# Kernel tuning notes

Measured on AMD Instinct MI355X. Metric: run time of the kernel, lower is better.

The kernel has to match this reference:

```python
import jax, jax.numpy as jnp
import numpy as np

B, C, H, W = 64, 512, 8, 8
K = 100            # num_class
H1, HID, L = 64, 128, 32   # ae_hidden[0], fixed hidd, ae_latent
CLIP = 100.0       # CSSRClassifier.clip_len
RED = -0.1         # model='pcssr' -> -1, times gamma=0.1
PUSH_THRESH = 10000.0


def setup_inputs() -> dict:
    key = jax.random.key(0)
    ks = jax.random.split(key, 9)
    s = lambda fan_in: 1.0 / np.sqrt(fan_in)  # kaiming-ish 1x1 conv init scale
    return {
        "x": jax.random.normal(ks[0], (B, C, H, W), jnp.float32),
        "ycls": jax.random.randint(ks[1], (B,), 0, K),
        "safe_margin_all": jax.random.normal(ks[2], (K,), jnp.float32),
        "safe_distance_all": jax.random.normal(ks[3], (K,), jnp.float32),
        "W1": jax.random.normal(ks[4], (K, H1, C), jnp.float32) * s(C),
        "W2": jax.random.normal(ks[5], (K, HID, H1), jnp.float32) * s(H1),
        "W3": jax.random.normal(ks[6], (K, L, HID), jnp.float32) * s(HID),
        "prototypes": jax.random.normal(ks[7], (K, L, H, W), jnp.float32),
        "prototypes1": jax.random.normal(ks[8], (K, L, H, W), jnp.float32),
    }


def reference(x, ycls, safe_margin_all, safe_distance_all, W1, W2, W3, prototypes, prototypes1):
    P = H * W
    xf = x.reshape(B, C, P)
    # per-class 1x1-conv encoder (tanh after every conv), batched over classes k
    h = jnp.tanh(jnp.einsum('koc,bcp->kbop', W1, xf))      # [K,B,H1,P]
    h = jnp.tanh(jnp.einsum('koi,kbip->kbop', W2, h))      # [K,B,HID,P]
    lt = jnp.tanh(jnp.einsum('koi,kbip->kbop', W3, h))     # [K,B,L,P]
    p = prototypes.reshape(K, 1, L, P)
    p1 = prototypes1.reshape(K, 1, L, P)
    # squared-L2 distance over channel dim, scaled by reduction, clipped
    er = jnp.clip(jnp.sum((lt - p) ** 2, axis=2) * RED, -CLIP, CLIP)    # [K,B,P]
    er1 = jnp.clip(jnp.sum((lt - p1) ** 2, axis=2) * RED, -CLIP, CLIP)  # [K,B,P]
    # training losses (pull on er1, push on er), vectorized across classes
    f = jnp.sum(er, axis=2)    # [K,B] spatial-summed errors
    f1 = jnp.sum(er1, axis=2)  # [K,B]
    cls_ids = jnp.arange(K)[:, None]
    mask_eq = (ycls[None, :] == cls_ids).astype(f.dtype)   # [K,B]
    n_eq = jnp.sum(mask_eq, axis=1)
    pull = jnp.sum(jnp.where(n_eq > 0,
                             jnp.sum(f1 * mask_eq, axis=1) / jnp.maximum(n_eq, 1.0),
                             0.0))
    comb = (1.0 - mask_eq) * (f < PUSH_THRESH).astype(f.dtype)
    n_comb = jnp.sum(comb, axis=1)
    push = jnp.sum(jnp.where(n_comb > 0,
                             jnp.sum(f * comb, axis=1) / jnp.maximum(n_comb, 1.0),
                             0.0))
    # cat per-class [B,1,H,W] errors along dim 1 -> [B,K,H,W]
    logits = jnp.transpose(er, (1, 0, 2)).reshape(B, K, H, W)
    logits1 = jnp.transpose(er1, (1, 0, 2)).reshape(B, K, H, W)
    return logits, logits1, pull, push
```

## Files before the change

kernel.cpp:

```cpp
#include <hip/hip_runtime.h>

typedef short  s16x8  __attribute__((ext_vector_type(8)));
typedef float  f32x16 __attribute__((ext_vector_type(16)));
typedef unsigned short u16;
typedef unsigned long long u64b;

#define MFMA32(a,b,c) __builtin_amdgcn_mfma_f32_32x32x16_bf16((a),(b),(c),0,0,0)
#define KCLS 100

__device__ __forceinline__ u16 f2bf(float f) {
  return (u16)(__builtin_bit_cast(unsigned, f) >> 16);
}

__device__ __forceinline__ float tanh_fast(float x) {
  float e = __builtin_amdgcn_exp2f(x * 2.8853900817779268f);
  return 1.0f - 2.0f * __builtin_amdgcn_rcpf(e + 1.0f);
}

__device__ __forceinline__ void ld_lds16(const void* g, void* l) {
  __builtin_amdgcn_global_load_lds(
      (const __attribute__((address_space(1))) unsigned char*)g,
      (__attribute__((address_space(3))) unsigned char*)l, 16, 0, 0);
}

__global__ void prep(const float* __restrict__ x, const float* __restrict__ w1,
                     const float* __restrict__ w2, const float* __restrict__ w3,
                     u16* __restrict__ xF, u16* __restrict__ W1F,
                     u16* __restrict__ W2F, u16* __restrict__ W3F,
                     float* __restrict__ fz, float* __restrict__ out2) {
  __shared__ float tile[64][65];
  const int bid = blockIdx.x, t = threadIdx.x;
  if (bid == 0 && t < 2) out2[t] = 0.f;
  if (bid < 512) {
    const int b = bid >> 3, ck = bid & 7;
    #pragma unroll
    for (int j = 0; j < 4; j++) {
      int e4 = j * 1024 + t * 4;
      int c = e4 >> 6, p0 = e4 & 63;
      float4 v = *(const float4*)(x + ((size_t)b * 512 + ck * 64 + c) * 64 + p0);
      tile[c][p0] = v.x; tile[c][p0 + 1] = v.y; tile[c][p0 + 2] = v.z; tile[c][p0 + 3] = v.w;
    }
    __syncthreads();
    #pragma unroll
    for (int i = 0; i < 2; i++) {
      int s = i * 256 + t;
      int ksl = s >> 7, ph = (s >> 6) & 1, lane = s & 63;
      int cb = ksl * 16 + (lane >> 5) * 8, pp = ph * 32 + (lane & 31);
      u16 o[8];
      #pragma unroll
      for (int jj = 0; jj < 8; jj++) o[jj] = f2bf(tile[cb + jj][pp]);
      *(uint4*)(xF + (((size_t)b * 64 + (ck * 4 + ksl) * 2 + ph) * 512) + lane * 8) = *(uint4*)o;
    }
  } else if (bid < 1312) {
    int base = (bid - 512) * 512;
    #pragma unroll
    for (int i = 0; i < 2; i++) {
      int s = base + i * 256 + t;
      int frag = s >> 6, lane = s & 63;
      int k = frag >> 6, fr = frag & 63;
      int m = (fr & 1) * 32 + (lane & 31);
      int c0 = (fr >> 1) * 16 + (lane >> 5) * 8;
      const float* src = w1 + ((size_t)k * 64 + m) * 512 + c0;
      float4 a = *(const float4*)src, b4 = *(const float4*)(src + 4);
      u16 o[8] = { f2bf(a.x), f2bf(a.y), f2bf(a.z), f2bf(a.w),
                   f2bf(b4.x), f2bf(b4.y), f2bf(b4.z), f2bf(b4.w) };
      *(uint4*)(W1F + ((size_t)frag * 512) + lane * 8) = *(uint4*)o;
    }
  } else if (bid < 1512) {
    int base = (bid - 1312) * 512;
    #pragma unroll
    for (int i = 0; i < 2; i++) {
      int s = base + i * 256 + t;
      int frag = s >> 6, lane = s & 63;
      int k = frag >> 4, fr = frag & 15;
      int m = (fr & 3) * 32 + (lane & 31);
      int c0 = (fr >> 2) * 16 + (lane >> 5) * 8;
      const float* src = w2 + ((size_t)k * 128 + m) * 64 + c0;
      float4 a = *(const float4*)src, b4 = *(const float4*)(src + 4);
      u16 o[8] = { f2bf(a.x), f2bf(a.y), f2bf(a.z), f2bf(a.w),
                   f2bf(b4.x), f2bf(b4.y), f2bf(b4.z), f2bf(b4.w) };
      *(uint4*)(W2F + ((size_t)frag * 512) + lane * 8) = *(uint4*)o;
    }
  } else if (bid < 1612) {
    int base = (bid - 1512) * 512;
    #pragma unroll
    for (int i = 0; i < 2; i++) {
      int s = base + i * 256 + t;
      int frag = s >> 6, lane = s & 63;
      int k = frag >> 3, kb = frag & 7;
      int m = lane & 31;
      int c0 = kb * 16 + (lane >> 5) * 8;
      const float* src = w3 + ((size_t)k * 32 + m) * 128 + c0;
      float4 a = *(const float4*)src, b4 = *(const float4*)(src + 4);
      u16 o[8] = { f2bf(a.x), f2bf(a.y), f2bf(a.z), f2bf(a.w),
                   f2bf(b4.x), f2bf(b4.y), f2bf(b4.z), f2bf(b4.w) };
      *(uint4*)(W3F + ((size_t)frag * 512) + lane * 8) = *(uint4*)o;
    }
  } else {
    int i4 = (bid - 1612) * 256 + t;
    if (i4 < 3200) {
      float4 z = {0.f, 0.f, 0.f, 0.f};
      *(float4*)(fz + (size_t)i4 * 4) = z;
    }
  }
}

__global__ __launch_bounds__(256, 4) void cssr_main(
    const u16* __restrict__ W1F, const u16* __restrict__ W2F, const u16* __restrict__ W3F,
    const u16* __restrict__ xF, const float* __restrict__ protos,
    const float* __restrict__ protos1, float* __restrict__ out,
    float* __restrict__ fw, float* __restrict__ f1w)
{
  __shared__ u16 pool[16384];

  const int bid = blockIdx.x;
  const int kp = bid >> 6, b = bid & 63;
  const int tid = threadIdx.x, w = tid >> 6, lane = tid & 63;
  const int nhalf = lane >> 5, nn = lane & 31;
  const int kk = w >> 1, mt = w & 1;
  const int k = kp * 2 + kk;

  const u16* xb = xF + ((size_t)b * 64) * 512;

  #pragma unroll
  for (int i = 0; i < 4; i++) {
    int f = w * 4 + i, gksl = f >> 1, ph = f & 1;
    ld_lds16(xb + ((size_t)(gksl * 2 + ph)) * 512 + lane * 8, &pool[f * 512]);
  }
  __syncthreads();

  f32x16 acc1[2] = {};
  for (int ci = 0; ci < 4; ci++) {
    const int pb = ci & 1;
    if (ci < 3) {
      #pragma unroll
      for (int i = 0; i < 4; i++) {
        int f = w * 4 + i, gksl = f >> 1, ph = f & 1;
        ld_lds16(xb + ((size_t)(((ci + 1) * 8 + gksl) * 2 + ph)) * 512 + lane * 8,
                 &pool[(pb ^ 1) * 8192 + f * 512]);
      }
    }
    #pragma unroll
    for (int ksl = 0; ksl < 8; ksl++) {
      s16x8 A = *(const s16x8*)(W1F + (((size_t)k * 64 + (ci * 8 + ksl) * 2 + mt) * 512) + lane * 8);
      #pragma unroll
      for (int nt = 0; nt < 2; nt++) {
        s16x8 B = *(const s16x8*)&pool[pb * 8192 + (ksl * 2 + nt) * 512 + lane * 8];
        acc1[nt] = MFMA32(A, B, acc1[nt]);
      }
    }
    __syncthreads();
  }

  #pragma unroll
  for (int nt = 0; nt < 2; nt++) {
    #pragma unroll
    for (int g = 0; g < 4; g++) {
      u16 hv[4];
      #pragma unroll
      for (int q = 0; q < 4; q++) hv[q] = f2bf(tanh_fast(acc1[nt][g * 4 + q]));
      int kb = mt * 2 + (g >> 1);
      int tl = (g & 1) * 32 + nn;
      *(u64b*)&pool[kk * 4096 + (kb * 2 + nt) * 512 + tl * 8 + nhalf * 4] = *(u64b*)hv;
    }
  }
  __syncthreads();

  f32x16 acc2[2][2] = {};
  #pragma unroll
  for (int kb = 0; kb < 4; kb++) {
    s16x8 A0 = *(const s16x8*)(W2F + (((size_t)k * 16 + kb * 4 + mt * 2 + 0) * 512) + lane * 8);
    s16x8 A1 = *(const s16x8*)(W2F + (((size_t)k * 16 + kb * 4 + mt * 2 + 1) * 512) + lane * 8);
    #pragma unroll
    for (int nh = 0; nh < 2; nh++) {
      s16x8 B = *(const s16x8*)&pool[kk * 4096 + (kb * 2 + nh) * 512 + lane * 8];
      acc2[0][nh] = MFMA32(A0, B, acc2[0][nh]);
      acc2[1][nh] = MFMA32(A1, B, acc2[1][nh]);
    }
  }
  __syncthreads();

  #pragma unroll
  for (int m4l = 0; m4l < 2; m4l++) {
    #pragma unroll
    for (int nh = 0; nh < 2; nh++) {
      #pragma unroll
      for (int g = 0; g < 4; g++) {
        u16 hv[4];
        #pragma unroll
        for (int q = 0; q < 4; q++) hv[q] = f2bf(tanh_fast(acc2[m4l][nh][g * 4 + q]));
        int kb2 = mt * 4 + m4l * 2 + (g >> 1);
        int tl  = (g & 1) * 32 + nn;
        *(u64b*)&pool[kk * 8192 + (kb2 * 2 + nh) * 512 + tl * 8 + nhalf * 4] = *(u64b*)hv;
      }
    }
  }
  __syncthreads();

  f32x16 acc3 = {};
  #pragma unroll
  for (int kb = 0; kb < 8; kb++) {
    s16x8 A = *(const s16x8*)(W3F + (((size_t)k * 8 + kb) * 512) + lane * 8);
    s16x8 B = *(const s16x8*)&pool[kk * 8192 + (kb * 2 + mt) * 512 + lane * 8];
    acc3 = MFMA32(A, B, acc3);
  }

  const int p = mt * 32 + nn;
  const float* pr  = protos  + (size_t)k * 2048;
  const float* pr1 = protos1 + (size_t)k * 2048;
  float d2 = 0.f, d21 = 0.f;
  #pragma unroll
  for (int g = 0; g < 4; g++) {
    #pragma unroll
    for (int q = 0; q < 4; q++) {
      int m = q + 8 * g + 4 * nhalf;
      float lt = tanh_fast(acc3[g * 4 + q]);
      float d = lt - pr [m * 64 + p];  d2  += d * d;
      float e = lt - pr1[m * 64 + p];  d21 += e * e;
    }
  }
  d2 += __shfl_xor(d2, 32); d21 += __shfl_xor(d21, 32);
  float er  = fminf(fmaxf(d2  * -0.1f, -100.f), 100.f);
  float er1 = fminf(fmaxf(d21 * -0.1f, -100.f), 100.f);
  if (nhalf == 0) {
    out[(size_t)b * 6400 + k * 64 + p]          = er;
    out[409600 + (size_t)b * 6400 + k * 64 + p] = er1;
  }
  float s = er, s1 = er1;
  s += __shfl_xor(s, 1);  s1 += __shfl_xor(s1, 1);
  s += __shfl_xor(s, 2);  s1 += __shfl_xor(s1, 2);
  s += __shfl_xor(s, 4);  s1 += __shfl_xor(s1, 4);
  s += __shfl_xor(s, 8);  s1 += __shfl_xor(s1, 8);
  s += __shfl_xor(s, 16); s1 += __shfl_xor(s1, 16);
  if (lane == 0) {
    atomicAdd(&fw [k * 64 + b], s);
    atomicAdd(&f1w[k * 64 + b], s1);
  }
}

__global__ void finalize(const float* __restrict__ f, const float* __restrict__ f1,
                         const int* __restrict__ ycls, float* __restrict__ out2) {
  const int k = blockIdx.x, b = threadIdx.x;
  float fv = f[k * 64 + b], f1v = f1[k * 64 + b];
  bool eq = (ycls[b] == k);
  bool cb = (!eq) && (fv < 10000.f);
  float s1 = eq ? f1v : 0.f, ne = eq ? 1.f : 0.f;
  float s  = cb ? fv  : 0.f, nc = cb ? 1.f : 0.f;
  #pragma unroll
  for (int o = 1; o < 64; o <<= 1) {
    s1 += __shfl_xor(s1, o); ne += __shfl_xor(ne, o);
    s  += __shfl_xor(s,  o); nc += __shfl_xor(nc, o);
  }
  if (b == 0) {
    if (ne > 0.f) atomicAdd(&out2[0], s1 / ne);
    if (nc > 0.f) atomicAdd(&out2[1], s / nc);
  }
}

extern "C" void kernel_launch(void* const* d_in, const int* in_sizes, int n_in,
                              void* d_out, int out_size, void* d_ws, size_t ws_size,
                              hipStream_t stream) {
  const float* x     = (const float*)d_in[0];
  const int*   ycls  = (const int*)d_in[1];
  const float* W1    = (const float*)d_in[4];
  const float* W2    = (const float*)d_in[5];
  const float* W3    = (const float*)d_in[6];
  const float* prot  = (const float*)d_in[7];
  const float* prot1 = (const float*)d_in[8];
  float* out = (float*)d_out;

  char* ws = (char*)d_ws;
  u16*  xFb = (u16*)(ws);
  u16*  W1F = (u16*)(ws + 4194304);
  u16*  W2F = (u16*)(ws + 10747904);
  u16*  W3F = (u16*)(ws + 12386304);
  float* fw  = (float*)(ws + 13205504);
  float* f1w = (float*)(ws + 13231104);

  prep<<<1625, 256, 0, stream>>>(x, W1, W2, W3, xFb, W1F, W2F, W3F,
                                 fw, out + 819200);
  cssr_main<<<50 * 64, 256, 0, stream>>>(W1F, W2F, W3F, xFb, prot, prot1,
                                         out, fw, f1w);
  finalize<<<KCLS, 64, 0, stream>>>(fw, f1w, ycls, out + 819200);
}
```

Before: 146.8 us.

## Keep inter-layer activations in registers via permlane32 swap, drop LDS staging

The main kernel is restructured so each wave owns one class, one batch item and half the spatial positions. The tanh outputs of layers 1 and 2 are packed to bf16 and rearranged into MFMA B-operand fragments with v_permlane32_swap, replacing the LDS round-trips and the block barriers between layers. The x tile is now read straight from global memory instead of being double-buffered through LDS, and the grid becomes 100x32 blocks. In exchange, W1 and x fragments are re-read from global/L2 by more waves, and register pressure rises.

After: 150.7 us. 1.03x slower.

```diff
diff --git a/kernel.cpp b/kernel.cpp
--- a/kernel.cpp
+++ b/kernel.cpp
@@ -3,6 +3,7 @@
 typedef short  s16x8  __attribute__((ext_vector_type(8)));
 typedef float  f32x16 __attribute__((ext_vector_type(16)));
 typedef unsigned short u16;
+typedef unsigned int   u32;
 typedef unsigned long long u64b;
 
 #define MFMA32(a,b,c) __builtin_amdgcn_mfma_f32_32x32x16_bf16((a),(b),(c),0,0,0)
@@ -10,17 +11,15 @@
 
 __device__ __forceinline__ u16 f2bf(float f) {
   return (u16)(__builtin_bit_cast(unsigned, f) >> 16);
+}
+
+__device__ __forceinline__ u32 pk2bf(float lo, float hi) {
+  return (__builtin_bit_cast(u32, lo) >> 16) | (__builtin_bit_cast(u32, hi) & 0xffff0000u);
 }
 
 __device__ __forceinline__ float tanh_fast(float x) {
   float e = __builtin_amdgcn_exp2f(x * 2.8853900817779268f);
   return 1.0f - 2.0f * __builtin_amdgcn_rcpf(e + 1.0f);
-}
-
-__device__ __forceinline__ void ld_lds16(const void* g, void* l) {
-  __builtin_amdgcn_global_load_lds(
-      (const __attribute__((address_space(1))) unsigned char*)g,
-      (__attribute__((address_space(3))) unsigned char*)l, 16, 0, 0);
 }
 
 __global__ void prep(const float* __restrict__ x, const float* __restrict__ w1,
@@ -105,124 +104,91 @@
   }
 }
 
+template<int GG>
+__device__ __forceinline__ s16x8 mk_bfrag(const f32x16 a) {
+  u32 P0 = pk2bf(tanh_fast(a[8 * GG + 0]), tanh_fast(a[8 * GG + 1]));
+  u32 P1 = pk2bf(tanh_fast(a[8 * GG + 2]), tanh_fast(a[8 * GG + 3]));
+  u32 Q0 = pk2bf(tanh_fast(a[8 * GG + 4]), tanh_fast(a[8 * GG + 5]));
+  u32 Q1 = pk2bf(tanh_fast(a[8 * GG + 6]), tanh_fast(a[8 * GG + 7]));
+  asm("v_permlane32_swap_b32 %0, %1" : "+v"(P0), "+v"(Q0));
+  asm("v_permlane32_swap_b32 %0, %1" : "+v"(P1), "+v"(Q1));
+  int4 wv = { (int)P0, (int)P1, (int)Q0, (int)Q1 };
+  return __builtin_bit_cast(s16x8, wv);
+}
+
 __global__ __launch_bounds__(256, 4) void cssr_main(
     const u16* __restrict__ W1F, const u16* __restrict__ W2F, const u16* __restrict__ W3F,
     const u16* __restrict__ xF, const float* __restrict__ protos,
     const float* __restrict__ protos1, float* __restrict__ out,
     float* __restrict__ fw, float* __restrict__ f1w)
 {
-  __shared__ u16 pool[16384];
-
   const int bid = blockIdx.x;
-  const int kp = bid >> 6, b = bid & 63;
+  const int k = bid >> 5, bp = bid & 31;
   const int tid = threadIdx.x, w = tid >> 6, lane = tid & 63;
-  const int nhalf = lane >> 5, nn = lane & 31;
-  const int kk = w >> 1, mt = w & 1;
-  const int k = kp * 2 + kk;
-
-  const u16* xb = xF + ((size_t)b * 64) * 512;
-
-  #pragma unroll
-  for (int i = 0; i < 4; i++) {
-    int f = w * 4 + i, gksl = f >> 1, ph = f & 1;
-    ld_lds16(xb + ((size_t)(gksl * 2 + ph)) * 512 + lane * 8, &pool[f * 512]);
-  }
-  __syncthreads();
+  const int bq = w >> 1, ph = w & 1;
+  const int b = bp * 2 + bq;
+  const int h = lane >> 5, nn = lane & 31;
+
+  const u16* xb  = xF  + ((size_t)b * 64) * 512 + lane * 8;
+  const u16* Wk1 = W1F + ((size_t)k * 64) * 512 + lane * 8;
 
   f32x16 acc1[2] = {};
-  for (int ci = 0; ci < 4; ci++) {
-    const int pb = ci & 1;
-    if (ci < 3) {
-      #pragma unroll
-      for (int i = 0; i < 4; i++) {
-        int f = w * 4 + i, gksl = f >> 1, ph = f & 1;
-        ld_lds16(xb + ((size_t)(((ci + 1) * 8 + gksl) * 2 + ph)) * 512 + lane * 8,
-                 &pool[(pb ^ 1) * 8192 + f * 512]);
-      }
-    }
-    #pragma unroll
-    for (int ksl = 0; ksl < 8; ksl++) {
-      s16x8 A = *(const s16x8*)(W1F + (((size_t)k * 64 + (ci * 8 + ksl) * 2 + mt) * 512) + lane * 8);
-      #pragma unroll
-      for (int nt = 0; nt < 2; nt++) {
-        s16x8 B = *(const s16x8*)&pool[pb * 8192 + (ksl * 2 + nt) * 512 + lane * 8];
-        acc1[nt] = MFMA32(A, B, acc1[nt]);
-      }
-    }
-    __syncthreads();
-  }
-
-  #pragma unroll
-  for (int nt = 0; nt < 2; nt++) {
-    #pragma unroll
-    for (int g = 0; g < 4; g++) {
-      u16 hv[4];
-      #pragma unroll
-      for (int q = 0; q < 4; q++) hv[q] = f2bf(tanh_fast(acc1[nt][g * 4 + q]));
-      int kb = mt * 2 + (g >> 1);
-      int tl = (g & 1) * 32 + nn;
-      *(u64b*)&pool[kk * 4096 + (kb * 2 + nt) * 512 + tl * 8 + nhalf * 4] = *(u64b*)hv;
-    }
-  }
-  __syncthreads();
-
-  f32x16 acc2[2][2] = {};
+  #pragma unroll
+  for (int ksl = 0; ksl < 32; ksl++) {
+    s16x8 B  = *(const s16x8*)(xb  + (ksl * 2 + ph) * 512);
+    s16x8 A0 = *(const s16x8*)(Wk1 + (ksl * 2 + 0) * 512);
+    s16x8 A1 = *(const s16x8*)(Wk1 + (ksl * 2 + 1) * 512);
+    acc1[0] = MFMA32(A0, B, acc1[0]);
+    acc1[1] = MFMA32(A1, B, acc1[1]);
+  }
+
+  s16x8 b1[4];
+  b1[0] = mk_bfrag<0>(acc1[0]); b1[1] = mk_bfrag<1>(acc1[0]);
+  b1[2] = mk_bfrag<0>(acc1[1]); b1[3] = mk_bfrag<1>(acc1[1]);
+
+  const u16* Wk2 = W2F + ((size_t)k * 16) * 512 + lane * 8;
+  f32x16 acc2[4] = {};
   #pragma unroll
   for (int kb = 0; kb < 4; kb++) {
-    s16x8 A0 = *(const s16x8*)(W2F + (((size_t)k * 16 + kb * 4 + mt * 2 + 0) * 512) + lane * 8);
-    s16x8 A1 = *(const s16x8*)(W2F + (((size_t)k * 16 + kb * 4 + mt * 2 + 1) * 512) + lane * 8);
-    #pragma unroll
-    for (int nh = 0; nh < 2; nh++) {
-      s16x8 B = *(const s16x8*)&pool[kk * 4096 + (kb * 2 + nh) * 512 + lane * 8];
-      acc2[0][nh] = MFMA32(A0, B, acc2[0][nh]);
-      acc2[1][nh] = MFMA32(A1, B, acc2[1][nh]);
-    }
-  }
-  __syncthreads();
-
-  #pragma unroll
-  for (int m4l = 0; m4l < 2; m4l++) {
-    #pragma unroll
-    for (int nh = 0; nh < 2; nh++) {
-      #pragma unroll
-      for (int g = 0; g < 4; g++) {
-        u16 hv[4];
-        #pragma unroll
-        for (int q = 0; q < 4; q++) hv[q] = f2bf(tanh_fast(acc2[m4l][nh][g * 4 + q]));
-        int kb2 = mt * 4 + m4l * 2 + (g >> 1);
-        int tl  = (g & 1) * 32 + nn;
-        *(u64b*)&pool[kk * 8192 + (kb2 * 2 + nh) * 512 + tl * 8 + nhalf * 4] = *(u64b*)hv;
-      }
-    }
-  }
-  __syncthreads();
-
+    #pragma unroll
+    for (int m4 = 0; m4 < 4; m4++) {
+      s16x8 A = *(const s16x8*)(Wk2 + (kb * 4 + m4) * 512);
+      acc2[m4] = MFMA32(A, b1[kb], acc2[m4]);
+    }
+  }
+
+  s16x8 b2[8];
+  b2[0] = mk_bfrag<0>(acc2[0]); b2[1] = mk_bfrag<1>(acc2[0]);
+  b2[2] = mk_bfrag<0>(acc2[1]); b2[3] = mk_bfrag<1>(acc2[1]);
+  b2[4] = mk_bfrag<0>(acc2[2]); b2[5] = mk_bfrag<1>(acc2[2]);
+  b2[6] = mk_bfrag<0>(acc2[3]); b2[7] = mk_bfrag<1>(acc2[3]);
+
+  const u16* Wk3 = W3F + ((size_t)k * 8) * 512 + lane * 8;
   f32x16 acc3 = {};
   #pragma unroll
   for (int kb = 0; kb < 8; kb++) {
-    s16x8 A = *(const s16x8*)(W3F + (((size_t)k * 8 + kb) * 512) + lane * 8);
-    s16x8 B = *(const s16x8*)&pool[kk * 8192 + (kb * 2 + mt) * 512 + lane * 8];
-    acc3 = MFMA32(A, B, acc3);
-  }
-
-  const int p = mt * 32 + nn;
-  const float* pr  = protos  + (size_t)k * 2048;
-  const float* pr1 = protos1 + (size_t)k * 2048;
+    s16x8 A = *(const s16x8*)(Wk3 + kb * 512);
+    acc3 = MFMA32(A, b2[kb], acc3);
+  }
+
+  const int p = ph * 32 + nn;
+  const float* pr  = protos  + (size_t)k * 2048 + p;
+  const float* pr1 = protos1 + (size_t)k * 2048 + p;
   float d2 = 0.f, d21 = 0.f;
   #pragma unroll
   for (int g = 0; g < 4; g++) {
     #pragma unroll
     for (int q = 0; q < 4; q++) {
-      int m = q + 8 * g + 4 * nhalf;
+      int m = q + 8 * g + 4 * h;
       float lt = tanh_fast(acc3[g * 4 + q]);
-      float d = lt - pr [m * 64 + p];  d2  += d * d;
-      float e = lt - pr1[m * 64 + p];  d21 += e * e;
+      float d = lt - pr [m * 64];  d2  += d * d;
+      float e = lt - pr1[m * 64];  d21 += e * e;
     }
   }
   d2 += __shfl_xor(d2, 32); d21 += __shfl_xor(d21, 32);
   float er  = fminf(fmaxf(d2  * -0.1f, -100.f), 100.f);
   float er1 = fminf(fmaxf(d21 * -0.1f, -100.f), 100.f);
-  if (nhalf == 0) {
+  if (h == 0) {
     out[(size_t)b * 6400 + k * 64 + p]          = er;
     out[409600 + (size_t)b * 6400 + k * 64 + p] = er1;
   }
@@ -279,7 +245,7 @@
 
   prep<<<1625, 256, 0, stream>>>(x, W1, W2, W3, xFb, W1F, W2F, W3F,
                                  fw, out + 819200);
-  cssr_main<<<50 * 64, 256, 0, stream>>>(W1F, W2F, W3F, xFb, prot, prot1,
-                                         out, fw, f1w);
+  cssr_main<<<KCLS * 32, 256, 0, stream>>>(W1F, W2F, W3F, xFb, prot, prot1,
+                                           out, fw, f1w);
   finalize<<<KCLS, 64, 0, stream>>>(fw, f1w, ycls, out + 819200);
 }
```
